# Kernel optimization log

Measured on AMD Instinct MI355X. Metric: run time of the kernel, lower is better.

## Reference

```python
import jax, jax.numpy as jnp
import numpy as np

# Model dims (match init_kwargs)
B, S, DIN, DIM = 1, 4096, 1024, 1024
NH, NKV = 16, 4
HD = DIM // NH          # head_dim = 64
GS = NH // NKV          # group_size = 4 (query heads per KV group)


def setup_inputs() -> dict:
    key = jax.random.key(0)
    ks = jax.random.split(key, 5)
    def w(k, shape, fan_in):
        return jax.random.normal(k, shape, jnp.float32) * (fan_in ** -0.5)
    return {
        "x": jax.random.normal(ks[0], (B, S, DIN), jnp.float32),
        "wq": w(ks[1], (DIM, DIN), DIN),            # nn.Linear(din, dim)
        "wk": w(ks[2], (NKV * HD, DIN), DIN),       # nn.Linear(din, nkv*hd)
        "wv": w(ks[3], (NKV * HD, DIN), DIN),
        "wo": w(ks[4], (DIM, DIM), DIM),            # output proj
    }


def reference(x, wq, wk, wv, wo):
    b, s, _ = x.shape
    # Projections (Linear: x @ W^T, bias=False)
    # Query head h = g*GS + m uses KV group g -> reshape heads as (g, m),
    # which is exactly repeat_interleave(group_size) on K/V without copying.
    q = (x @ wq.T).reshape(b, s, NKV, GS, HD)   # [b, s, g, m, d]
    k = (x @ wk.T).reshape(b, s, NKV, HD)       # [b, s, g, d]
    v = (x @ wv.T).reshape(b, s, NKV, HD)
    scale = jnp.asarray(HD ** 0.5, x.dtype)
    att = jnp.einsum('bsgmd,btgd->bgmst', q, k) / scale  # [b, g, m, s, s]
    causal = jnp.triu(jnp.ones((s, s), bool), 1)
    att = jnp.where(causal, -jnp.inf, att)
    att = jax.nn.softmax(att, axis=-1)          # dropout p=0.0 -> identity
    ctx = jnp.einsum('bgmst,btgd->bsgmd', att, v).reshape(b, s, DIM)
    return ctx @ wo.T
```

## Files before the change

### kernel.cpp

```cpp
#include <hip/hip_runtime.h>

typedef __bf16 bf16_t;
typedef __bf16 bf16x8 __attribute__((ext_vector_type(8)));
typedef float  f32x4  __attribute__((ext_vector_type(4)));

#define MFMA16(a, b, c) __builtin_amdgcn_mfma_f32_16x16x32_bf16((a), (b), (c), 0, 0, 0)

__device__ __forceinline__ void gload_lds16(const void* g, void* l) {
  __builtin_amdgcn_global_load_lds((__attribute__((address_space(1))) void*)(g),
                                   (__attribute__((address_space(3))) void*)(l),
                                   16, 0, 0);
}

__global__ __launch_bounds__(256) void cvt_all(const float* __restrict__ x,
                                               const float* __restrict__ wq,
                                               const float* __restrict__ wk,
                                               const float* __restrict__ wv,
                                               const float* __restrict__ wo,
                                               bf16_t* __restrict__ xb,
                                               bf16_t* __restrict__ wqkv,
                                               bf16_t* __restrict__ wob) {
  int i = (blockIdx.x * 256 + threadIdx.x) * 8;
  const float* src;
  bf16_t* dst;
  int off;
  if (i < 4194304)      { src = x;  dst = xb;             off = i; }
  else if (i < 5242880) { src = wq; dst = wqkv;           off = i - 4194304; }
  else if (i < 5505024) { src = wk; dst = wqkv + 1048576; off = i - 5242880; }
  else if (i < 5767168) { src = wv; dst = wqkv + 1310720; off = i - 5505024; }
  else                  { src = wo; dst = wob;            off = i - 5767168; }
  const float4* pp = reinterpret_cast<const float4*>(src + off);
  float4 a = pp[0], b = pp[1];
  bf16x8 v;
  v[0] = (bf16_t)a.x; v[1] = (bf16_t)a.y; v[2] = (bf16_t)a.z; v[3] = (bf16_t)a.w;
  v[4] = (bf16_t)b.x; v[5] = (bf16_t)b.y; v[6] = (bf16_t)b.z; v[7] = (bf16_t)b.w;
  *reinterpret_cast<bf16x8*>(dst + off) = v;
}

template <typename T>
__global__ __launch_bounds__(256) void gemm_bt(const bf16_t* __restrict__ A,
                                               const bf16_t* __restrict__ B,
                                               T* __restrict__ C,
                                               int M, int N, int K,
                                               bf16_t* __restrict__ kp,
                                               bf16_t* __restrict__ vt) {
  constexpr int BK = 64;
  int tid  = threadIdx.x;
  int lane = tid & 63, w = tid >> 6;
  int wr = w >> 1, wc = w & 1;
  int l15 = lane & 15, lhi = lane >> 4;
  int row0 = blockIdx.y * 128, col0 = blockIdx.x * 128;

  __shared__ alignas(16) char smem[128 * BK * 2 * 2];
  char* sA = smem;
  char* sB = smem + 128 * BK * 2;

  f32x4 acc[4][4] = {};

  for (int k0 = 0; k0 < K; k0 += BK) {
#pragma unroll
    for (int i = 0; i < 4; ++i) {
      int c = i * 256 + tid;
      int r = c >> 3, kc = c & 7;
      int kk = k0 + ((kc ^ (r & 7)) << 3);
      gload_lds16(A + (size_t)(row0 + r) * K + kk, sA + c * 16);
      gload_lds16(B + (size_t)(col0 + r) * K + kk, sB + c * 16);
    }
    __syncthreads();
#pragma unroll
    for (int s = 0; s < 2; ++s) {
      bf16x8 af[4], bfr[4];
#pragma unroll
      for (int mi = 0; mi < 4; ++mi) {
        int r = wr * 64 + mi * 16 + l15;
        af[mi] = *reinterpret_cast<const bf16x8*>(
            sA + r * 128 + (((s * 4 + lhi) ^ (r & 7)) << 4));
      }
#pragma unroll
      for (int nj = 0; nj < 4; ++nj) {
        int r = wc * 64 + nj * 16 + l15;
        bfr[nj] = *reinterpret_cast<const bf16x8*>(
            sB + r * 128 + (((s * 4 + lhi) ^ (r & 7)) << 4));
      }
#pragma unroll
      for (int mi = 0; mi < 4; ++mi)
#pragma unroll
        for (int nj = 0; nj < 4; ++nj)
          acc[mi][nj] = MFMA16(af[mi], bfr[nj], acc[mi][nj]);
    }
    __syncthreads();
  }

  const float KSCALE = 0.18033688f;
#pragma unroll
  for (int mi = 0; mi < 4; ++mi)
#pragma unroll
    for (int nj = 0; nj < 4; ++nj) {
      int colb = col0 + wc * 64 + nj * 16 + l15;
      int rowb = row0 + wr * 64 + mi * 16 + lhi * 4;
      if (kp != nullptr && colb >= 1024) {
        if (colb < 1280) {
          int gg = (colb - 1024) >> 6, d = (colb - 1024) & 63;
          bf16_t* kdst = kp + ((size_t)gg * 4096 + rowb) * 64 + d;
#pragma unroll
          for (int r2 = 0; r2 < 4; ++r2)
            kdst[r2 * 64] = (bf16_t)(acc[mi][nj][r2] * KSCALE);
        } else {
          union { bf16_t hh[4]; uint64_t u; } a;
#pragma unroll
          for (int r2 = 0; r2 < 4; ++r2) a.hh[r2] = (bf16_t)acc[mi][nj][r2];
          *reinterpret_cast<uint64_t*>(vt + (size_t)(colb - 1280) * 4096 + rowb) = a.u;
        }
      } else {
#pragma unroll
        for (int r2 = 0; r2 < 4; ++r2)
          C[(size_t)(rowb + r2) * N + colb] = (T)acc[mi][nj][r2];
      }
    }
}

__global__ __launch_bounds__(256, 2) void attn_kernel(const bf16_t* __restrict__ qkv,
                                                      const bf16_t* __restrict__ kp,
                                                      const bf16_t* __restrict__ vt,
                                                      bf16_t* __restrict__ ctx,
                                                      float* __restrict__ Opart,
                                                      float* __restrict__ lpart) {
  int tid = threadIdx.x, lane = tid & 63, w = tid >> 6;
  int l15 = lane & 15, lhi = lane >> 4;
  int e = l15 & 7;
  int bid = blockIdx.x;
  int pos = bid & 15, qq = bid >> 4;
  int p = qq >> 1, half = qq & 1;
  int g = (pos & 7) >> 1;
  int h = g * 4 + (((pos >> 3) << 1) | (pos & 1));

  __shared__ alignas(16) char kv[2][16384];
  __shared__ alignas(16) char pb_all[4][2048];
  char* pbuf = pb_all[w];

  const bf16_t* kbase = kp + (size_t)g * 4096 * 64;
  const bf16_t* vbase = vt + (size_t)g * 64 * 4096;

  auto STAGE = [&](int j0, int b) {
#pragma unroll
    for (int i = 0; i < 2; ++i) {
      int c = i * 256 + tid;
      int r = c >> 3, kc = c & 7;
      int d8 = kc ^ (r & 7);
      gload_lds16(kbase + (size_t)(j0 + r) * 64 + d8 * 8, &kv[b][c * 16]);
    }
#pragma unroll
    for (int i = 0; i < 2; ++i) {
      int c = i * 256 + tid;
      int r = c >> 3, kc = c & 7;
      int d8 = kc ^ (r & 7);
      gload_lds16(vbase + (size_t)r * 4096 + j0 + d8 * 8, &kv[b][8192 + c * 16]);
    }
  };

  auto runPhase = [&](int tile, int sbeg, int send, bool fin,
                      float* Oslot, float* lslot) {
    int r0 = tile * 64;
    int wr0 = r0 + w * 16;

    bf16x8 qf[2];
#pragma unroll
    for (int ks = 0; ks < 2; ++ks)
      qf[ks] = *reinterpret_cast<const bf16x8*>(
          qkv + (size_t)(wr0 + l15) * 1536 + h * 64 + ks * 32 + lhi * 8);

    f32x4 O[4] = {};
    float lsum = 0.f;

    STAGE(sbeg * 64, 0);
    __syncthreads();

    for (int step = sbeg; step < send; ++step) {
      int b = (step - sbeg) & 1;
      if (step + 1 < send) STAGE((step + 1) * 64, b ^ 1);
      int j0 = step * 64;
      const char* kt  = kv[b];
      const char* vtl = kv[b] + 8192;
      bool diag = (j0 + 64 > r0);
#pragma unroll
      for (int nj = 0; nj < 4; ++nj) {
        int kr = nj * 16 + l15;
        const char* krow = kt + kr * 128;
        bf16x8 k0 = *reinterpret_cast<const bf16x8*>(krow + ((lhi ^ (kr & 7)) << 4));
        bf16x8 k1 = *reinterpret_cast<const bf16x8*>(krow + (((4 + lhi) ^ (kr & 7)) << 4));
        f32x4 t = {0.f, 0.f, 0.f, 0.f};
        t = MFMA16(k0, qf[0], t);
        t = MFMA16(k1, qf[1], t);
        if (diag) {
          int qr = wr0 + l15;
#pragma unroll
          for (int r = 0; r < 4; ++r) {
            int key = j0 + nj * 16 + lhi * 4 + r;
            if (key > qr) t[r] = -1e30f;
          }
        }
        int sw = (nj * 2 + (lhi >> 1)) ^ e;
        union { bf16_t hh[4]; uint64_t u; } a;
        float ls = 0.f;
#pragma unroll
        for (int r = 0; r < 4; ++r) {
          float pv = exp2f(t[r]);
          ls += pv;
          a.hh[r] = (bf16_t)pv;
        }
        lsum += ls;
        *reinterpret_cast<uint64_t*>(pbuf + l15 * 128 + sw * 16 + ((lhi & 1) << 3)) = a.u;
      }
      bf16x8 ap[2];
#pragma unroll
      for (int ks = 0; ks < 2; ++ks)
        ap[ks] = *reinterpret_cast<const bf16x8*>(
            pbuf + l15 * 128 + (((ks * 4 + lhi) ^ e) << 4));
#pragma unroll
      for (int h4 = 0; h4 < 4; ++h4) {
        int vr = h4 * 16 + l15;
        const char* vrow = vtl + vr * 128;
        bf16x8 v0 = *reinterpret_cast<const bf16x8*>(vrow + ((lhi ^ (vr & 7)) << 4));
        bf16x8 v1 = *reinterpret_cast<const bf16x8*>(vrow + (((4 + lhi) ^ (vr & 7)) << 4));
        O[h4] = MFMA16(ap[0], v0, O[h4]);
        O[h4] = MFMA16(ap[1], v1, O[h4]);
      }
      __syncthreads();
    }

    lsum += __shfl_xor(lsum, 16);
    lsum += __shfl_xor(lsum, 32);
    if (fin) {
      float il[4];
#pragma unroll
      for (int r = 0; r < 4; ++r)
        il[r] = 1.0f / __shfl(lsum, lhi * 4 + r);
#pragma unroll
      for (int h4 = 0; h4 < 4; ++h4)
#pragma unroll
        for (int r = 0; r < 4; ++r) {
          int row = wr0 + lhi * 4 + r;
          ctx[(size_t)row * 1024 + h * 64 + h4 * 16 + l15] =
              (bf16_t)(O[h4][r] * il[r]);
        }
    } else {
      if (lhi == 0) lslot[w * 16 + l15] = lsum;
#pragma unroll
      for (int h4 = 0; h4 < 4; ++h4)
#pragma unroll
        for (int r = 0; r < 4; ++r)
          Oslot[(size_t)(w * 16 + lhi * 4 + r) * 64 + h4 * 16 + l15] = O[h4][r];
    }
  };

  if (half == 0) {
    bool fin = (p == 31);
    if (fin) {
      runPhase(63 - p, 0, 33, true, nullptr, nullptr);
    } else {
      int u = (30 - p) * 16 + h;
      runPhase(63 - p, 0, 33, false,
               Opart + ((size_t)u * 2 + 0) * 4096, lpart + ((size_t)u * 2 + 0) * 64);
    }
  } else {
    if (p < 31) {
      int u = (30 - p) * 16 + h;
      runPhase(63 - p, 33, 64 - p, false,
               Opart + ((size_t)u * 2 + 1) * 4096, lpart + ((size_t)u * 2 + 1) * 64);
    }
    runPhase(p, 0, p + 1, true, nullptr, nullptr);
  }
}

__global__ __launch_bounds__(256) void norm_combine(const float* __restrict__ Opart,
                                                    const float* __restrict__ lpart,
                                                    bf16_t* __restrict__ ctx) {
  int u = blockIdx.x;
  int T = 33 + (u >> 4), h = u & 15;
  int t = threadIdx.x;
  int row = t >> 2, q = t & 3;
  const float* O0 = Opart + (size_t)u * 2 * 4096;
  const float* O1 = O0 + 4096;
  const float* l0 = lpart + (size_t)u * 2 * 64;
  const float* l1 = l0 + 64;
  float il = 1.0f / (l0[row] + l1[row]);
#pragma unroll
  for (int i = 0; i < 4; ++i) {
    int idx = row * 64 + q * 16 + i * 4;
    f32x4 a = *reinterpret_cast<const f32x4*>(O0 + idx);
    f32x4 b = *reinterpret_cast<const f32x4*>(O1 + idx);
    union { bf16_t hh[4]; uint64_t uu; } o;
#pragma unroll
    for (int r = 0; r < 4; ++r) o.hh[r] = (bf16_t)((a[r] + b[r]) * il);
    *reinterpret_cast<uint64_t*>(
        ctx + (size_t)(T * 64 + row) * 1024 + h * 64 + q * 16 + i * 4) = o.uu;
  }
}

extern "C" void kernel_launch(void* const* d_in, const int* in_sizes, int n_in,
                              void* d_out, int out_size, void* d_ws, size_t ws_size,
                              hipStream_t stream) {
  const float* x  = (const float*)d_in[0];
  const float* wq = (const float*)d_in[1];
  const float* wk = (const float*)d_in[2];
  const float* wv = (const float*)d_in[3];
  const float* wo = (const float*)d_in[4];
  float* out = (float*)d_out;

  char* ws = (char*)d_ws;
  size_t off = 0;
  auto alloc = [&](size_t b) {
    char* p = ws + off;
    off += (b + 255) & ~(size_t)255;
    return p;
  };
  bf16_t* wob  = (bf16_t*)alloc((size_t)1024 * 1024 * 2);
  bf16_t* qkv  = (bf16_t*)alloc((size_t)4096 * 1536 * 2);
  bf16_t* vtb  = (bf16_t*)alloc((size_t)256 * 4096 * 2);
  bf16_t* kpb  = (bf16_t*)alloc((size_t)4 * 4096 * 64 * 2);
  bf16_t* ctx  = (bf16_t*)alloc((size_t)4096 * 1024 * 2);
  size_t scratch_base = off;
  bf16_t* xb   = (bf16_t*)alloc((size_t)4096 * 1024 * 2);
  bf16_t* wqkv = (bf16_t*)alloc((size_t)1536 * 1024 * 2);
  float* Opart = (float*)(ws + scratch_base);
  float* lpart = Opart + (size_t)496 * 2 * 4096;

  cvt_all<<<3328, 256, 0, stream>>>(x, wq, wk, wv, wo, xb, wqkv, wob);
  gemm_bt<bf16_t><<<dim3(12, 32), 256, 0, stream>>>(xb, wqkv, qkv, 4096, 1536, 1024,
                                                    kpb, vtb);
  attn_kernel<<<1024, 256, 0, stream>>>(qkv, kpb, vtb, ctx, Opart, lpart);
  norm_combine<<<496, 256, 0, stream>>>(Opart, lpart, ctx);
  gemm_bt<float><<<dim3(8, 32), 256, 0, stream>>>(ctx, wob, out, 4096, 1024, 1024,
                                                  nullptr, nullptr);
}
```

Measured before the change: 127.5 us.

## Halve attention key tile to 32 and skip fully masked per-wave tiles

The attention loop now stages 32 keys per step instead of 64, with a re-swizzled half-size V tile and a smaller P buffer. Each wave skips the MFMA work for key tiles that lie entirely above its 16 causal rows. The split of work between block halves is rebalanced so every long tile is split into two partials, which the combine kernel now handles for 512 units. The aim is to cut wasted masked compute on the diagonal and to shrink LDS use, at the cost of twice as many steps and barriers, each doing less MFMA work.

```diff
diff --git a/kernel.cpp b/kernel.cpp
--- a/kernel.cpp
+++ b/kernel.cpp
@@ -127,34 +127,31 @@
                                                       float* __restrict__ lpart) {
   int tid = threadIdx.x, lane = tid & 63, w = tid >> 6;
   int l15 = lane & 15, lhi = lane >> 4;
-  int e = l15 & 7;
   int bid = blockIdx.x;
   int pos = bid & 15, qq = bid >> 4;
   int p = qq >> 1, half = qq & 1;
   int g = (pos & 7) >> 1;
   int h = g * 4 + (((pos >> 3) << 1) | (pos & 1));
 
-  __shared__ alignas(16) char kv[2][16384];
-  __shared__ alignas(16) char pb_all[4][2048];
+  __shared__ alignas(16) char kv[2][8192];
+  __shared__ alignas(16) char pb_all[4][1280];
   char* pbuf = pb_all[w];
 
   const bf16_t* kbase = kp + (size_t)g * 4096 * 64;
   const bf16_t* vbase = vt + (size_t)g * 64 * 4096;
 
   auto STAGE = [&](int j0, int b) {
-#pragma unroll
-    for (int i = 0; i < 2; ++i) {
-      int c = i * 256 + tid;
+    {
+      int c = tid;
       int r = c >> 3, kc = c & 7;
       int d8 = kc ^ (r & 7);
       gload_lds16(kbase + (size_t)(j0 + r) * 64 + d8 * 8, &kv[b][c * 16]);
     }
-#pragma unroll
-    for (int i = 0; i < 2; ++i) {
-      int c = i * 256 + tid;
-      int r = c >> 3, kc = c & 7;
-      int d8 = kc ^ (r & 7);
-      gload_lds16(vbase + (size_t)r * 4096 + j0 + d8 * 8, &kv[b][8192 + c * 16]);
+    {
+      int c = tid;
+      int hd = c >> 2, kc = c & 3;
+      int k8 = kc ^ (hd & 3);
+      gload_lds16(vbase + (size_t)hd * 4096 + j0 + k8 * 8, &kv[b][4096 + c * 16]);
     }
   };
 
@@ -172,58 +169,53 @@
     f32x4 O[4] = {};
     float lsum = 0.f;
 
-    STAGE(sbeg * 64, 0);
+    STAGE(sbeg * 32, 0);
     __syncthreads();
 
     for (int step = sbeg; step < send; ++step) {
       int b = (step - sbeg) & 1;
-      if (step + 1 < send) STAGE((step + 1) * 64, b ^ 1);
-      int j0 = step * 64;
-      const char* kt  = kv[b];
-      const char* vtl = kv[b] + 8192;
-      bool diag = (j0 + 64 > r0);
-#pragma unroll
-      for (int nj = 0; nj < 4; ++nj) {
-        int kr = nj * 16 + l15;
-        const char* krow = kt + kr * 128;
-        bf16x8 k0 = *reinterpret_cast<const bf16x8*>(krow + ((lhi ^ (kr & 7)) << 4));
-        bf16x8 k1 = *reinterpret_cast<const bf16x8*>(krow + (((4 + lhi) ^ (kr & 7)) << 4));
-        f32x4 t = {0.f, 0.f, 0.f, 0.f};
-        t = MFMA16(k0, qf[0], t);
-        t = MFMA16(k1, qf[1], t);
-        if (diag) {
-          int qr = wr0 + l15;
+      if (step + 1 < send) STAGE((step + 1) * 32, b ^ 1);
+      int j0 = step * 32;
+      if (j0 <= wr0 + 15) {
+        const char* kt  = kv[b];
+        const char* vtl = kv[b] + 4096;
+        bool diag = (j0 + 32 > wr0);
+#pragma unroll
+        for (int nj = 0; nj < 2; ++nj) {
+          int kr = nj * 16 + l15;
+          const char* krow = kt + kr * 128;
+          bf16x8 k0 = *reinterpret_cast<const bf16x8*>(krow + ((lhi ^ (kr & 7)) << 4));
+          bf16x8 k1 = *reinterpret_cast<const bf16x8*>(krow + (((4 + lhi) ^ (kr & 7)) << 4));
+          f32x4 t = {0.f, 0.f, 0.f, 0.f};
+          t = MFMA16(k0, qf[0], t);
+          t = MFMA16(k1, qf[1], t);
+          if (diag) {
+            int qr = wr0 + l15;
+#pragma unroll
+            for (int r = 0; r < 4; ++r) {
+              int key = j0 + nj * 16 + lhi * 4 + r;
+              if (key > qr) t[r] = -1e30f;
+            }
+          }
+          union { bf16_t hh[4]; uint64_t u; } a;
+          float ls = 0.f;
 #pragma unroll
           for (int r = 0; r < 4; ++r) {
-            int key = j0 + nj * 16 + lhi * 4 + r;
-            if (key > qr) t[r] = -1e30f;
+            float pv = exp2f(t[r]);
+            ls += pv;
+            a.hh[r] = (bf16_t)pv;
           }
+          lsum += ls;
+          *reinterpret_cast<uint64_t*>(pbuf + l15 * 80 + nj * 32 + lhi * 8) = a.u;
         }
-        int sw = (nj * 2 + (lhi >> 1)) ^ e;
-        union { bf16_t hh[4]; uint64_t u; } a;
-        float ls = 0.f;
-#pragma unroll
-        for (int r = 0; r < 4; ++r) {
-          float pv = exp2f(t[r]);
-          ls += pv;
-          a.hh[r] = (bf16_t)pv;
+        bf16x8 ap = *reinterpret_cast<const bf16x8*>(pbuf + l15 * 80 + lhi * 16);
+#pragma unroll
+        for (int h4 = 0; h4 < 4; ++h4) {
+          int vr = h4 * 16 + l15;
+          const char* vrow = vtl + vr * 64;
+          bf16x8 v0 = *reinterpret_cast<const bf16x8*>(vrow + ((lhi ^ (vr & 3)) << 4));
+          O[h4] = MFMA16(ap, v0, O[h4]);
         }
-        lsum += ls;
-        *reinterpret_cast<uint64_t*>(pbuf + l15 * 128 + sw * 16 + ((lhi & 1) << 3)) = a.u;
-      }
-      bf16x8 ap[2];
-#pragma unroll
-      for (int ks = 0; ks < 2; ++ks)
-        ap[ks] = *reinterpret_cast<const bf16x8*>(
-            pbuf + l15 * 128 + (((ks * 4 + lhi) ^ e) << 4));
-#pragma unroll
-      for (int h4 = 0; h4 < 4; ++h4) {
-        int vr = h4 * 16 + l15;
-        const char* vrow = vtl + vr * 128;
-        bf16x8 v0 = *reinterpret_cast<const bf16x8*>(vrow + ((lhi ^ (vr & 7)) << 4));
-        bf16x8 v1 = *reinterpret_cast<const bf16x8*>(vrow + (((4 + lhi) ^ (vr & 7)) << 4));
-        O[h4] = MFMA16(ap[0], v0, O[h4]);
-        O[h4] = MFMA16(ap[1], v1, O[h4]);
       }
       __syncthreads();
     }
@@ -253,22 +245,15 @@
     }
   };
 
+  int T1 = 63 - p;
+  int u = (31 - p) * 16 + h;
   if (half == 0) {
-    bool fin = (p == 31);
-    if (fin) {
-      runPhase(63 - p, 0, 33, true, nullptr, nullptr);
-    } else {
-      int u = (30 - p) * 16 + h;
-      runPhase(63 - p, 0, 33, false,
-               Opart + ((size_t)u * 2 + 0) * 4096, lpart + ((size_t)u * 2 + 0) * 64);
-    }
+    runPhase(T1, 0, 65, false,
+             Opart + ((size_t)u * 2 + 0) * 4096, lpart + ((size_t)u * 2 + 0) * 64);
   } else {
-    if (p < 31) {
-      int u = (30 - p) * 16 + h;
-      runPhase(63 - p, 33, 64 - p, false,
-               Opart + ((size_t)u * 2 + 1) * 4096, lpart + ((size_t)u * 2 + 1) * 64);
-    }
-    runPhase(p, 0, p + 1, true, nullptr, nullptr);
+    runPhase(T1, 65, 128 - 2 * p, false,
+             Opart + ((size_t)u * 2 + 1) * 4096, lpart + ((size_t)u * 2 + 1) * 64);
+    runPhase(p, 0, 2 * p + 2, true, nullptr, nullptr);
   }
 }
 
@@ -276,7 +261,7 @@
                                                     const float* __restrict__ lpart,
                                                     bf16_t* __restrict__ ctx) {
   int u = blockIdx.x;
-  int T = 33 + (u >> 4), h = u & 15;
+  int T = 32 + (u >> 4), h = u & 15;
   int t = threadIdx.x;
   int row = t >> 2, q = t & 3;
   const float* O0 = Opart + (size_t)u * 2 * 4096;
@@ -323,13 +308,13 @@
   bf16_t* xb   = (bf16_t*)alloc((size_t)4096 * 1024 * 2);
   bf16_t* wqkv = (bf16_t*)alloc((size_t)1536 * 1024 * 2);
   float* Opart = (float*)(ws + scratch_base);
-  float* lpart = Opart + (size_t)496 * 2 * 4096;
+  float* lpart = Opart + (size_t)512 * 2 * 4096;
 
   cvt_all<<<3328, 256, 0, stream>>>(x, wq, wk, wv, wo, xb, wqkv, wob);
   gemm_bt<bf16_t><<<dim3(12, 32), 256, 0, stream>>>(xb, wqkv, qkv, 4096, 1536, 1024,
                                                     kpb, vtb);
   attn_kernel<<<1024, 256, 0, stream>>>(qkv, kpb, vtb, ctx, Opart, lpart);
-  norm_combine<<<496, 256, 0, stream>>>(Opart, lpart, ctx);
+  norm_combine<<<512, 256, 0, stream>>>(Opart, lpart, ctx);
   gemm_bt<float><<<dim3(8, 32), 256, 0, stream>>>(ctx, wob, out, 4096, 1024, 1024,
                                                   nullptr, nullptr);
 }
```

Result: slower. 133.9 us (+5.1%).

## Rebalance causal attention into 768 equal-work blocks and compute row sums via MFMA

Applied to the files above, without the earlier changes.

Replaces the 1024-block scheme, where each block handled up to two phases for a pair of query tiles, with 768 blocks. Each block takes an equal third (43 steps) of a four-tile chain covering pairs of long and short causal tiles, and tiles split across a boundary write partials that norm_combine merges. The softmax denominator is now accumulated by an MFMA against a ones vector instead of scalar adds and cross-lane shuffles. The partition adds index logic and up to two partial-tile phases per block, and the combine kernel launches 512 blocks, some of which exit early.

```diff
diff --git a/kernel.cpp b/kernel.cpp
--- a/kernel.cpp
+++ b/kernel.cpp
@@ -129,8 +129,9 @@
   int l15 = lane & 15, lhi = lane >> 4;
   int e = l15 & 7;
   int bid = blockIdx.x;
-  int pos = bid & 15, qq = bid >> 4;
-  int p = qq >> 1, half = qq & 1;
+  int pos = bid & 15;
+  int gb = bid >> 4;
+  int i = gb / 3, k = gb - i * 3;
   int g = (pos & 7) >> 1;
   int h = g * 4 + (((pos >> 3) << 1) | (pos & 1));
 
@@ -143,20 +144,24 @@
 
   auto STAGE = [&](int j0, int b) {
 #pragma unroll
-    for (int i = 0; i < 2; ++i) {
-      int c = i * 256 + tid;
+    for (int ii = 0; ii < 2; ++ii) {
+      int c = ii * 256 + tid;
       int r = c >> 3, kc = c & 7;
       int d8 = kc ^ (r & 7);
       gload_lds16(kbase + (size_t)(j0 + r) * 64 + d8 * 8, &kv[b][c * 16]);
     }
 #pragma unroll
-    for (int i = 0; i < 2; ++i) {
-      int c = i * 256 + tid;
+    for (int ii = 0; ii < 2; ++ii) {
+      int c = ii * 256 + tid;
       int r = c >> 3, kc = c & 7;
       int d8 = kc ^ (r & 7);
       gload_lds16(vbase + (size_t)r * 4096 + j0 + d8 * 8, &kv[b][8192 + c * 16]);
     }
   };
+
+  bf16x8 ones;
+#pragma unroll
+  for (int ii = 0; ii < 8; ++ii) ones[ii] = (bf16_t)1.0f;
 
   auto runPhase = [&](int tile, int sbeg, int send, bool fin,
                       float* Oslot, float* lslot) {
@@ -170,7 +175,7 @@
           qkv + (size_t)(wr0 + l15) * 1536 + h * 64 + ks * 32 + lhi * 8);
 
     f32x4 O[4] = {};
-    float lsum = 0.f;
+    f32x4 lacc = {0.f, 0.f, 0.f, 0.f};
 
     STAGE(sbeg * 64, 0);
     __syncthreads();
@@ -201,14 +206,8 @@
         }
         int sw = (nj * 2 + (lhi >> 1)) ^ e;
         union { bf16_t hh[4]; uint64_t u; } a;
-        float ls = 0.f;
-#pragma unroll
-        for (int r = 0; r < 4; ++r) {
-          float pv = exp2f(t[r]);
-          ls += pv;
-          a.hh[r] = (bf16_t)pv;
-        }
-        lsum += ls;
+#pragma unroll
+        for (int r = 0; r < 4; ++r) a.hh[r] = (bf16_t)exp2f(t[r]);
         *reinterpret_cast<uint64_t*>(pbuf + l15 * 128 + sw * 16 + ((lhi & 1) << 3)) = a.u;
       }
       bf16x8 ap[2];
@@ -216,6 +215,8 @@
       for (int ks = 0; ks < 2; ++ks)
         ap[ks] = *reinterpret_cast<const bf16x8*>(
             pbuf + l15 * 128 + (((ks * 4 + lhi) ^ e) << 4));
+      lacc = MFMA16(ap[0], ones, lacc);
+      lacc = MFMA16(ap[1], ones, lacc);
 #pragma unroll
       for (int h4 = 0; h4 < 4; ++h4) {
         int vr = h4 * 16 + l15;
@@ -228,23 +229,20 @@
       __syncthreads();
     }
 
-    lsum += __shfl_xor(lsum, 16);
-    lsum += __shfl_xor(lsum, 32);
     if (fin) {
-      float il[4];
-#pragma unroll
-      for (int r = 0; r < 4; ++r)
-        il[r] = 1.0f / __shfl(lsum, lhi * 4 + r);
 #pragma unroll
       for (int h4 = 0; h4 < 4; ++h4)
 #pragma unroll
         for (int r = 0; r < 4; ++r) {
           int row = wr0 + lhi * 4 + r;
           ctx[(size_t)row * 1024 + h * 64 + h4 * 16 + l15] =
-              (bf16_t)(O[h4][r] * il[r]);
+              (bf16_t)(O[h4][r] / lacc[r]);
         }
     } else {
-      if (lhi == 0) lslot[w * 16 + l15] = lsum;
+      if (l15 == 0) {
+#pragma unroll
+        for (int r = 0; r < 4; ++r) lslot[w * 16 + lhi * 4 + r] = lacc[r];
+      }
 #pragma unroll
       for (int h4 = 0; h4 < 4; ++h4)
 #pragma unroll
@@ -253,22 +251,31 @@
     }
   };
 
-  if (half == 0) {
-    bool fin = (p == 31);
-    if (fin) {
-      runPhase(63 - p, 0, 33, true, nullptr, nullptr);
-    } else {
-      int u = (30 - p) * 16 + h;
-      runPhase(63 - p, 0, 33, false,
-               Opart + ((size_t)u * 2 + 0) * 4096, lpart + ((size_t)u * 2 + 0) * 64);
-    }
-  } else {
-    if (p < 31) {
-      int u = (30 - p) * 16 + h;
-      runPhase(63 - p, 33, 64 - p, false,
-               Opart + ((size_t)u * 2 + 1) * 4096, lpart + ((size_t)u * 2 + 1) * 64);
-    }
-    runPhase(p, 0, p + 1, true, nullptr, nullptr);
+  int s0 = (k == 0) ? 0 : (k == 1 ? 43 : 86);
+  int s1 = (k == 0) ? 43 : (k == 1 ? 86 : 130);
+  int tiles[4] = {63 - 2 * i, 2 * i, 62 - 2 * i, 2 * i + 1};
+  int lens[4]  = {64 - 2 * i, 2 * i + 1, 63 - 2 * i, 2 * i + 2};
+  int st = 0;
+#pragma unroll
+  for (int t = 0; t < 4; ++t) {
+    int tb = st, te = st + lens[t];
+    st = te;
+    int a = s0 > tb ? s0 : tb;
+    int b2 = s1 < te ? s1 : te;
+    if (a < b2) {
+      int sbeg = a - tb, send = b2 - tb;
+      bool fin = (sbeg == 0 && send == lens[t]);
+      if (fin) {
+        runPhase(tiles[t], 0, lens[t], true, nullptr, nullptr);
+      } else {
+        int bnd = (sbeg > 0) ? (k - 1) : k;
+        int c = (sbeg == 0) ? 0 : 1;
+        int slotu = (i * 2 + bnd) * 16 + h;
+        runPhase(tiles[t], sbeg, send, false,
+                 Opart + ((size_t)slotu * 2 + c) * 4096,
+                 lpart + ((size_t)slotu * 2 + c) * 64);
+      }
+    }
   }
 }
 
@@ -276,24 +283,38 @@
                                                     const float* __restrict__ lpart,
                                                     bf16_t* __restrict__ ctx) {
   int u = blockIdx.x;
-  int T = 33 + (u >> 4), h = u & 15;
-  int t = threadIdx.x;
-  int row = t >> 2, q = t & 3;
-  const float* O0 = Opart + (size_t)u * 2 * 4096;
+  int bidx = u & 1;
+  int hi = u >> 1;
+  int h = hi & 15, i = hi >> 4;
+  int tiles[4] = {63 - 2 * i, 2 * i, 62 - 2 * i, 2 * i + 1};
+  int lens[4]  = {64 - 2 * i, 2 * i + 1, 63 - 2 * i, 2 * i + 2};
+  int s = bidx ? 86 : 43;
+  int T = -1, st = 0;
+#pragma unroll
+  for (int t = 0; t < 4; ++t) {
+    if (st < s && s < st + lens[t]) T = tiles[t];
+    st += lens[t];
+  }
+  if (T < 0) return;
+  int slotu = (i * 2 + bidx) * 16 + h;
+
+  int tt = threadIdx.x;
+  int row = tt >> 2, q = tt & 3;
+  const float* O0 = Opart + (size_t)slotu * 2 * 4096;
   const float* O1 = O0 + 4096;
-  const float* l0 = lpart + (size_t)u * 2 * 64;
+  const float* l0 = lpart + (size_t)slotu * 2 * 64;
   const float* l1 = l0 + 64;
   float il = 1.0f / (l0[row] + l1[row]);
 #pragma unroll
-  for (int i = 0; i < 4; ++i) {
-    int idx = row * 64 + q * 16 + i * 4;
+  for (int ii = 0; ii < 4; ++ii) {
+    int idx = row * 64 + q * 16 + ii * 4;
     f32x4 a = *reinterpret_cast<const f32x4*>(O0 + idx);
     f32x4 b = *reinterpret_cast<const f32x4*>(O1 + idx);
     union { bf16_t hh[4]; uint64_t uu; } o;
 #pragma unroll
     for (int r = 0; r < 4; ++r) o.hh[r] = (bf16_t)((a[r] + b[r]) * il);
     *reinterpret_cast<uint64_t*>(
-        ctx + (size_t)(T * 64 + row) * 1024 + h * 64 + q * 16 + i * 4) = o.uu;
+        ctx + (size_t)(T * 64 + row) * 1024 + h * 64 + q * 16 + ii * 4) = o.uu;
   }
 }
 
@@ -323,13 +344,13 @@
   bf16_t* xb   = (bf16_t*)alloc((size_t)4096 * 1024 * 2);
   bf16_t* wqkv = (bf16_t*)alloc((size_t)1536 * 1024 * 2);
   float* Opart = (float*)(ws + scratch_base);
-  float* lpart = Opart + (size_t)496 * 2 * 4096;
+  float* lpart = Opart + (size_t)512 * 2 * 4096;
 
   cvt_all<<<3328, 256, 0, stream>>>(x, wq, wk, wv, wo, xb, wqkv, wob);
   gemm_bt<bf16_t><<<dim3(12, 32), 256, 0, stream>>>(xb, wqkv, qkv, 4096, 1536, 1024,
                                                     kpb, vtb);
-  attn_kernel<<<1024, 256, 0, stream>>>(qkv, kpb, vtb, ctx, Opart, lpart);
-  norm_combine<<<496, 256, 0, stream>>>(Opart, lpart, ctx);
+  attn_kernel<<<768, 256, 0, stream>>>(qkv, kpb, vtb, ctx, Opart, lpart);
+  norm_combine<<<512, 256, 0, stream>>>(Opart, lpart, ctx);
   gemm_bt<float><<<dim3(8, 32), 256, 0, stream>>>(ctx, wob, out, 4096, 1024, 1024,
                                                   nullptr, nullptr);
 }
```

After: 130.7 us. 1.03x slower.
